# Optimization experiments

Hardware: AMD Instinct MI355X
Metric: run time of the kernel (lower is better)

The kernel has to match this reference:

```python
import jax, jax.numpy as jnp
import numpy as np

D_MODEL = 2048
N_HEADS = 16
HEAD_DIM = D_MODEL // N_HEADS
ROPE_BASE = 10000.0


def rope(x):
    # x: [b, h, s, d]; matches the torch module exactly:
    # x1 = even dims, x2 = odd dims; output = concat([x1*cos - x2*sin, x1*sin + x2*cos], -1)
    b, h, s, d = x.shape
    theta = 1.0 / ROPE_BASE ** (jnp.arange(0, d, 2, dtype=jnp.float32) / d)  # [d/2]
    angles = jnp.arange(s, dtype=jnp.float32)[:, None] * theta[None, :]       # [s, d/2]
    cos = jnp.cos(angles)[None, None]  # [1,1,s,d/2]
    sin = jnp.sin(angles)[None, None]
    x1, x2 = x[..., ::2], x[..., 1::2]
    return jnp.concatenate([x1 * cos - x2 * sin, x1 * sin + x2 * cos], axis=-1)


def setup_inputs() -> dict:
    key = jax.random.key(0)
    ks = jax.random.split(key, 5)
    b, s = 2, 2048
    x = jax.random.normal(ks[0], (b, s, D_MODEL), dtype=jnp.float32)
    scale_in = 1.0 / np.sqrt(D_MODEL)
    Wqkv = jax.random.normal(ks[1], (D_MODEL, 3 * D_MODEL), dtype=jnp.float32) * scale_in
    bqkv = jnp.zeros((3 * D_MODEL,), dtype=jnp.float32)
    Wo = jax.random.normal(ks[2], (D_MODEL, D_MODEL), dtype=jnp.float32) * scale_in
    bo = jnp.zeros((D_MODEL,), dtype=jnp.float32)
    return {"x": x, "Wqkv": Wqkv, "bqkv": bqkv, "Wo": Wo, "bo": bo}


def reference(x, Wqkv, bqkv, Wo, bo):
    b, s, d = x.shape
    qkv = x @ Wqkv + bqkv                      # [b, s, 3d]
    q, k, v = jnp.split(qkv, 3, axis=-1)
    def to_heads(t):
        return t.reshape(b, s, N_HEADS, HEAD_DIM).transpose(0, 2, 1, 3)  # [b,h,s,hd]
    q, k, v = to_heads(q), to_heads(k), to_heads(v)
    q = rope(q)
    k = rope(k)
    scores = jnp.einsum('bhqd,bhkd->bhqk', q, k) / jnp.sqrt(jnp.float32(HEAD_DIM))
    attn = jax.nn.softmax(scores, axis=-1)
    out = jnp.einsum('bhqk,bhkd->bhqd', attn, v)
    out = out.transpose(0, 2, 1, 3).reshape(b, s, d)
    return out @ Wo + bo
```

## Files before the change

kernel.cpp:

```cpp
#include <hip/hip_runtime.h>
#include <hip/hip_bf16.h>
#include <cstdint>
#include <type_traits>

#define D_MODEL 2048
#define NH 16
#define HD 128
#define SEQ 2048
#define QKV_LD (3 * D_MODEL)

typedef __attribute__((ext_vector_type(8))) short short8;
typedef __attribute__((ext_vector_type(4))) float f32x4;
typedef __attribute__((ext_vector_type(16))) float f32x16;

__device__ __forceinline__ ushort f2bf(float f) {
    union { float f; uint32_t u; } c; c.f = f;
    uint32_t u = c.u;
    uint32_t r = (u + 0x7FFFu + ((u >> 16) & 1u)) >> 16;
    return (ushort)r;
}
__device__ __forceinline__ float bf2f(ushort b) {
    union { uint32_t u; float f; } c; c.u = ((uint32_t)b) << 16;
    return c.f;
}

__device__ __forceinline__ void load_lds16(const ushort* g, ushort* l) {
    __builtin_amdgcn_global_load_lds(
        (const __attribute__((address_space(1))) void*)g,
        (__attribute__((address_space(3))) void*)l, 16, 0, 0);
}

#define WAITV(N) asm volatile("s_waitcnt vmcnt(" #N ")" ::: "memory")
#define BARF()   do { __builtin_amdgcn_s_barrier(); \
                      asm volatile("" ::: "memory"); } while (0)
#define PRIO1    __builtin_amdgcn_s_setprio(1)
#define PRIO0    __builtin_amdgcn_s_setprio(0)

__global__ void cvt_bf16_kernel(const float* __restrict__ in, ushort* __restrict__ out, int n4) {
    int idx = blockIdx.x * blockDim.x + threadIdx.x;
    if (idx >= n4) return;
    float4 v = ((const float4*)in)[idx];
    ushort4 o;
    o.x = f2bf(v.x); o.y = f2bf(v.y); o.z = f2bf(v.z); o.w = f2bf(v.w);
    ((ushort4*)out)[idx] = o;
}

__global__ void transpose_bf16_kernel(const float* __restrict__ in, ushort* __restrict__ out,
                                      int R, int C) {
    __shared__ float tile[32][33];
    int tx = threadIdx.x, ty = threadIdx.y;
    int c0 = blockIdx.x * 32, r0 = blockIdx.y * 32;
    for (int i = 0; i < 4; ++i) {
        int r = r0 + ty + i * 8;
        tile[ty + i * 8][tx] = in[(size_t)r * C + c0 + tx];
    }
    __syncthreads();
    for (int i = 0; i < 4; ++i) {
        int c = c0 + ty + i * 8;
        out[(size_t)c * R + r0 + tx] = f2bf(tile[tx][ty + i * 8]);
    }
}

#define B_ROWOFF(L) (NHALF == 2 ? (((L) & 1) * 128 + ((L) >> 1) * 32) : ((L) * 64))
#define STAGE_A(L, T_, B_) load_lds16(Ag + (size_t)(L) * 64 * K + (size_t)(T_) * 64, \
                                      smA + (B_) * 16384 + (L) * 4096 + ldsW)
#define STAGE_B(L, T_, B_) load_lds16(Bg + (size_t)B_ROWOFF(L) * K + (size_t)(T_) * 64, \
                                      smB + (B_) * (8192 * NHALF) + (L) * 4096 + ldsW)
#define READ_A(MH) do { const ushort* _ab = smA + cb * 16384 + aRow + (MH) * 4096; \
    _Pragma("unroll") for (int i_ = 0; i_ < 4; ++i_) { \
        af[i_][0] = *(const short8*)(_ab + i_ * 1024 + pc0); \
        af[i_][1] = *(const short8*)(_ab + i_ * 1024 + pc1); } } while (0)
#define READ_BH(dst, NHh) do { const ushort* _bb = smB + cb * (8192 * NHALF) + (NHh) * 8192 + bRow; \
    _Pragma("unroll") for (int j_ = 0; j_ < 2; ++j_) { \
        dst[j_][0] = *(const short8*)(_bb + j_ * 1024 + pc0); \
        dst[j_][1] = *(const short8*)(_bb + j_ * 1024 + pc1); } } while (0)
#define MFMA_PH(MH, NHh, bf) do { \
    _Pragma("unroll") for (int i_ = 0; i_ < 4; ++i_) \
    _Pragma("unroll") for (int j_ = 0; j_ < 2; ++j_) { \
        acc[(MH) * 4 + i_][(NHh) * 2 + j_] = __builtin_amdgcn_mfma_f32_16x16x32_bf16( \
            af[i_][0], bf[j_][0], acc[(MH) * 4 + i_][(NHh) * 2 + j_], 0, 0, 0); \
        acc[(MH) * 4 + i_][(NHh) * 2 + j_] = __builtin_amdgcn_mfma_f32_16x16x32_bf16( \
            af[i_][1], bf[j_][1], acc[(MH) * 4 + i_][(NHh) * 2 + j_], 0, 0, 0); } } while (0)

template <typename OutT, int NHALF>
__global__ __launch_bounds__(512, 2) void gemm256(
    const ushort* __restrict__ A,
    const ushort* __restrict__ Bt,
    const float* __restrict__ bias,
    OutT* __restrict__ C,
    int M, int N, int K)
{
    __shared__ __align__(16) ushort sm[32768 + 2 * 8192 * NHALF];
    ushort* smA = sm;
    ushort* smB = sm + 32768;

    int t = threadIdx.x;
    int w = t >> 6, lane = t & 63;
    int lr = lane & 15, lh = lane >> 4;
    int wm_idx = w >> 2, wn_idx = w & 3;
    int m0 = blockIdx.y * 256, n0 = blockIdx.x * (128 * NHALF);

    int srow = t >> 3;
    int scol = ((t & 7) ^ (srow & 7)) << 3;
    const ushort* Ag = A + (size_t)(m0 + srow) * K + scol;
    int bq = (NHALF == 2) ? ((srow >> 5) * 64 + (srow & 31)) : srow;
    const ushort* Bg = Bt + (size_t)(n0 + bq) * K + scol;
    int ldsW = w * 512;

    int pc0 = (lh ^ (lr & 7)) << 3;
    int pc1 = ((4 + lh) ^ (lr & 7)) << 3;
    int aRow = (wm_idx * 128 + lr) * 64;
    int bRow = (wn_idx * 32 + lr) * 64;

    f32x4 acc[8][2 * NHALF];
#pragma unroll
    for (int i = 0; i < 8; ++i)
#pragma unroll
        for (int j = 0; j < 2 * NHALF; ++j) acc[i][j] = (f32x4)0.0f;
    short8 af[4][2], bf0[2][2], bf1[2][2];

    int NT = K >> 6;

    if constexpr (NHALF == 2) {
        STAGE_A(0, 0, 0); STAGE_A(2, 0, 0); STAGE_B(0, 0, 0); STAGE_B(1, 0, 0);
        STAGE_B(2, 0, 0); STAGE_B(3, 0, 0);
        STAGE_A(1, 0, 0); STAGE_A(3, 0, 0);
        WAITV(4);
    } else {
        STAGE_A(0, 0, 0); STAGE_A(2, 0, 0); STAGE_B(0, 0, 0);
        STAGE_B(1, 0, 0); STAGE_A(1, 0, 0); STAGE_A(3, 0, 0);
        WAITV(2);
    }
    BARF();

    for (int T = 0; T < NT; ++T) {
        int cb = T & 1, nb = cb ^ 1;
        bool pf = (T + 1 < NT);
        if constexpr (NHALF == 2) {
            READ_A(0); READ_BH(bf0, 0);
            if (pf) { STAGE_A(0, T + 1, nb); STAGE_A(2, T + 1, nb);
                      STAGE_B(0, T + 1, nb); STAGE_B(1, T + 1, nb); }
            BARF();
            PRIO1; MFMA_PH(0, 0, bf0); PRIO0;
            if (pf) WAITV(6); else WAITV(2);
            BARF();
            READ_BH(bf1, 1);
            if (pf) { STAGE_B(2, T + 1, nb); STAGE_B(3, T + 1, nb); }
            BARF();
            PRIO1; MFMA_PH(0, 1, bf1); PRIO0;
            if (pf) WAITV(6); else WAITV(0);
            BARF();
            READ_A(1);
            if (pf) { STAGE_A(1, T + 1, nb); STAGE_A(3, T + 1, nb); }
            BARF();
            PRIO1; MFMA_PH(1, 1, bf1); MFMA_PH(1, 0, bf0); PRIO0;
            if (pf) WAITV(4);
            BARF();
        } else {
            READ_A(0); READ_BH(bf0, 0);
            if (pf) { STAGE_A(0, T + 1, nb); STAGE_A(2, T + 1, nb); STAGE_B(0, T + 1, nb); }
            BARF();
            PRIO1; MFMA_PH(0, 0, bf0); PRIO0;
            if (pf) WAITV(3); else WAITV(0);
            BARF();
            READ_A(1);
            if (pf) { STAGE_B(1, T + 1, nb); STAGE_A(1, T + 1, nb); STAGE_A(3, T + 1, nb); }
            BARF();
            PRIO1; MFMA_PH(1, 0, bf0); PRIO0;
            if (pf) WAITV(2);
            BARF();
        }
    }

    float bv[2 * NHALF];
#pragma unroll
    for (int jj = 0; jj < 2 * NHALF; ++jj) bv[jj] = bias[n0 + wn_idx * 32 * NHALF + jj * 16 + lr];
#pragma unroll
    for (int ii = 0; ii < 8; ++ii) {
        int row = m0 + wm_idx * 128 + ii * 16 + lh * 4;
#pragma unroll
        for (int jj = 0; jj < 2 * NHALF; ++jj) {
            int col = n0 + wn_idx * 32 * NHALF + jj * 16 + lr;
#pragma unroll
            for (int r = 0; r < 4; ++r) {
                float v = acc[ii][jj][r] + bv[jj];
                if constexpr (std::is_same<OutT, ushort>::value)
                    C[(size_t)(row + r) * N + col] = f2bf(v);
                else
                    C[(size_t)(row + r) * N + col] = v;
            }
        }
    }
}

#define STAGE_A3(L, T_, B_) load_lds16(Ag + (size_t)(L) * 64 * K + (size_t)(T_) * 64, \
                                       smA + (B_) * 8192 + (L) * 4096 + ldsW)
#define STAGE_B3(L, T_, B_) load_lds16(Bg + (size_t)((((L) & 1) * 2 + wnp) * 96 + ((L) >> 1) * 32 + rb) * K + (size_t)(T_) * 64, \
                                       smB + (B_) * 24576 + (L) * 4096 + ldsW)
#define READ_A3() do { const ushort* _ab = smA + cb * 8192 + aRow; \
    _Pragma("unroll") for (int i_ = 0; i_ < 4; ++i_) { \
        af[i_][0] = *(const short8*)(_ab + i_ * 1024 + pc0); \
        af[i_][1] = *(const short8*)(_ab + i_ * 1024 + pc1); } } while (0)
#define READ_B3(H) do { const ushort* _bb = smB + cb * 24576 + (H) * 8192 + bRow; \
    _Pragma("unroll") for (int j_ = 0; j_ < 2; ++j_) { \
        bfr[j_][0] = *(const short8*)(_bb + j_ * 1024 + pc0); \
        bfr[j_][1] = *(const short8*)(_bb + j_ * 1024 + pc1); } } while (0)
#define MFMA_P3(H) do { \
    _Pragma("unroll") for (int i_ = 0; i_ < 4; ++i_) \
    _Pragma("unroll") for (int j_ = 0; j_ < 2; ++j_) { \
        acc[i_][(H) * 2 + j_] = __builtin_amdgcn_mfma_f32_16x16x32_bf16( \
            af[i_][0], bfr[j_][0], acc[i_][(H) * 2 + j_], 0, 0, 0); \
        acc[i_][(H) * 2 + j_] = __builtin_amdgcn_mfma_f32_16x16x32_bf16( \
            af[i_][1], bfr[j_][1], acc[i_][(H) * 2 + j_], 0, 0, 0); } } while (0)

__global__ __launch_bounds__(512, 2) void gemm384(
    const ushort* __restrict__ A,
    const ushort* __restrict__ Bt,
    const float* __restrict__ bias,
    ushort* __restrict__ C,
    int M, int N, int K)
{
    __shared__ __align__(16) ushort sm[65536];
    ushort* smA = sm;
    ushort* smB = sm + 16384;

    int t = threadIdx.x;
    int w = t >> 6, lane = t & 63;
    int lr = lane & 15, lh = lane >> 4;
    int wm_idx = w >> 2, wn_idx = w & 3;
    int m0 = blockIdx.y * 128, n0 = blockIdx.x * 384;

    int srow = t >> 3;
    int scol = ((t & 7) ^ (srow & 7)) << 3;
    const ushort* Ag = A + (size_t)(m0 + srow) * K + scol;
    const ushort* Bg = Bt + (size_t)n0 * K + scol;
    int wnp = srow >> 5;
    int rb = srow & 31;
    int ldsW = w * 512;

    int pc0 = (lh ^ (lr & 7)) << 3;
    int pc1 = ((4 + lh) ^ (lr & 7)) << 3;
    int aRow = (wm_idx * 64 + lr) * 64;
    int bRow = (wn_idx * 32 + lr) * 64;

    f32x4 acc[4][6];
#pragma unroll
    for (int i = 0; i < 4; ++i)
#pragma unroll
        for (int j = 0; j < 6; ++j) acc[i][j] = (f32x4)0.0f;
    short8 af[4][2], bfr[2][2];

    int NT = K >> 6;

    STAGE_A3(0, 0, 0); STAGE_A3(1, 0, 0); STAGE_B3(0, 0, 0); STAGE_B3(1, 0, 0);
    STAGE_B3(2, 0, 0); STAGE_B3(3, 0, 0); STAGE_B3(4, 0, 0); STAGE_B3(5, 0, 0);
    WAITV(4);
    BARF();

    for (int T = 0; T < NT; ++T) {
        int cb = T & 1, nb = cb ^ 1;
        bool pf = (T + 1 < NT);
        READ_A3(); READ_B3(0);
        if (pf) { STAGE_A3(0, T + 1, nb); STAGE_A3(1, T + 1, nb); STAGE_B3(0, T + 1, nb); }
        BARF();
        PRIO1; MFMA_P3(0); PRIO0;
        if (pf) WAITV(5); else WAITV(2);
        BARF();
        READ_B3(1);
        if (pf) { STAGE_B3(1, T + 1, nb); STAGE_B3(2, T + 1, nb); STAGE_B3(3, T + 1, nb); }
        BARF();
        PRIO1; MFMA_P3(1); PRIO0;
        if (pf) WAITV(6); else WAITV(0);
        BARF();
        READ_B3(2);
        if (pf) { STAGE_B3(4, T + 1, nb); STAGE_B3(5, T + 1, nb); }
        BARF();
        PRIO1; MFMA_P3(2); PRIO0;
        if (pf) WAITV(4);
        BARF();
    }

    float bv[6];
#pragma unroll
    for (int jj = 0; jj < 6; ++jj) bv[jj] = bias[n0 + wn_idx * 96 + jj * 16 + lr];
#pragma unroll
    for (int ii = 0; ii < 4; ++ii) {
        int row = m0 + wm_idx * 64 + ii * 16 + lh * 4;
#pragma unroll
        for (int jj = 0; jj < 6; ++jj) {
            int col = n0 + wn_idx * 96 + jj * 16 + lr;
#pragma unroll
            for (int r = 0; r < 4; ++r) {
                float v = acc[ii][jj][r] + bv[jj];
                C[(size_t)(row + r) * N + col] = f2bf(v);
            }
        }
    }
}

__global__ void rope_table(float2* __restrict__ tab) {
    int i = blockIdx.x * blockDim.x + threadIdx.x;
    int s = i >> 6, j = i & 63;
    float theta = powf(10000.0f, -(float)j * (1.0f / 64.0f));
    float ang = (float)s * theta;
    float sn, cs;
    sincosf(ang, &sn, &cs);
    tab[i] = make_float2(cs, sn);
}

__global__ void rope_cast_qk(const ushort* __restrict__ qkv,
                             const float2* __restrict__ tab,
                             ushort* __restrict__ Qb, ushort* __restrict__ Kb) {
    int t = threadIdx.x;
    int wv = blockIdx.x * 4 + (t >> 6);
    int j = t & 63;
    int bs = wv >> 5;
    int rem = wv & 31;
    int which = rem >> 4;
    int h = rem & 15;
    int s = bs & 2047;
    int b = bs >> 11;
    size_t src = (size_t)bs * QKV_LD + which * D_MODEL + h * HD;
    uint32_t pr = *(const uint32_t*)(qkv + src + 2 * j);
    float x1 = bf2f((ushort)(pr & 0xffff));
    float x2 = bf2f((ushort)(pr >> 16));
    float2 cspair = tab[(s << 6) + j];
    float cs = cspair.x, sn = cspair.y;
    float sc = which ? 1.0f : 0.08838834764831845f;
    float o1 = (x1 * cs - x2 * sn) * sc;
    float o2 = (x1 * sn + x2 * cs) * sc;
    ushort* dst = which ? Kb : Qb;
    size_t obase = ((size_t)(b * NH + h) * SEQ + s) * HD;
    dst[obase + j] = f2bf(o1);
    dst[obase + 64 + j] = f2bf(o2);
}

__global__ void v_transpose(const ushort* __restrict__ qkv, ushort* __restrict__ Vt) {
    __shared__ ushort tile[32][33];
    int tx = threadIdx.x, ty = threadIdx.y;
    int s0 = blockIdx.x * 32;
    int d0 = blockIdx.y * 32;
    int bh = blockIdx.z;
    int b = bh >> 4, h = bh & 15;
    for (int i = 0; i < 4; ++i) {
        int s = s0 + ty + i * 8;
        tile[ty + i * 8][tx] = qkv[((size_t)(b * SEQ + s)) * QKV_LD + 2 * D_MODEL + h * HD + d0 + tx];
    }
    __syncthreads();
    for (int i = 0; i < 4; ++i) {
        int d = d0 + ty + i * 8;
        Vt[((size_t)bh * HD + d) * SEQ + s0 + tx] = tile[tx][ty + i * 8];
    }
}

__global__ __launch_bounds__(256) void attn_mfma(const ushort* __restrict__ Qb,
                                                 const ushort* __restrict__ Kb,
                                                 const ushort* __restrict__ Vt,
                                                 ushort* __restrict__ ctx) {
    __shared__ ushort smem[25600];
    ushort* Ks = smem;
    ushort* Vts = smem + 8192;
    ushort* Ps = smem + 16384;

    int t = threadIdx.x;
    int w = t >> 6, l = t & 63;
    int l31 = l & 31, g = l >> 5;
    int q0 = blockIdx.x * 128;
    int bh = blockIdx.y;
    int b = bh >> 4, h = bh & 15;

    int qrow = q0 + w * 32 + l31;
    const ushort* Qg = Qb + ((size_t)bh * SEQ + qrow) * HD;
    short8 qf[8];
#pragma unroll
    for (int kc = 0; kc < 8; kc++)
        qf[kc] = *(const short8*)(Qg + kc * 16 + g * 8);

    f32x16 O[4];
#pragma unroll
    for (int di = 0; di < 4; di++) O[di] = (f32x16)0.0f;
    float m_run = -INFINITY, l_run = 0.0f;

    const ushort* KgB = Kb + (size_t)bh * SEQ * HD;
    const ushort* VtB = Vt + (size_t)bh * HD * SEQ;

    for (int k0 = 0; k0 < SEQ; k0 += 64) {
        __syncthreads();
#pragma unroll
        for (int c2 = 0; c2 < 4; c2++) {
            int f = c2 * 256 + t;
            int r = f >> 4, c = f & 15;
            int cp = c ^ (r & 15);
            uint4 v = *(const uint4*)(KgB + (size_t)(k0 + r) * HD + c * 8);
            *(uint4*)(Ks + r * 128 + cp * 8) = v;
        }
#pragma unroll
        for (int c2 = 0; c2 < 4; c2++) {
            int f = c2 * 256 + t;
            int d = f >> 3, c = f & 7;
            int cp = c ^ (d & 7);
            uint4 v = *(const uint4*)(VtB + (size_t)d * SEQ + k0 + c * 8);
            *(uint4*)(Vts + d * 64 + cp * 8) = v;
        }
        __syncthreads();

        f32x16 St[2];
        St[0] = (f32x16)0.0f;
        St[1] = (f32x16)0.0f;
        PRIO1;
#pragma unroll
        for (int ki = 0; ki < 2; ki++) {
            int row = ki * 32 + l31;
#pragma unroll
            for (int kc = 0; kc < 8; kc++) {
                int cp = (kc * 2 + g) ^ (row & 15);
                short8 a = *(const short8*)(Ks + row * 128 + cp * 8);
                St[ki] = __builtin_amdgcn_mfma_f32_32x32x16_bf16(a, qf[kc], St[ki], 0, 0, 0);
            }
        }
        PRIO0;

        float mx = -INFINITY;
#pragma unroll
        for (int ki = 0; ki < 2; ki++)
#pragma unroll
            for (int r = 0; r < 16; r++) mx = fmaxf(mx, St[ki][r]);
        mx = fmaxf(mx, __shfl_xor(mx, 32));
        float mn = fmaxf(m_run, mx);
        float alpha = __expf(m_run - mn);
        m_run = mn;
        float psum = 0.0f;
#pragma unroll
        for (int ki = 0; ki < 2; ki++)
#pragma unroll
            for (int r = 0; r < 16; r++) {
                float p = __expf(St[ki][r] - mn);
                St[ki][r] = p;
                psum += p;
            }
        psum += __shfl_xor(psum, 32);
        l_run = l_run * alpha + psum;
#pragma unroll
        for (int di = 0; di < 4; di++)
#pragma unroll
            for (int r = 0; r < 16; r++) O[di][r] *= alpha;

        {
            int qloc = w * 32 + l31;
            ushort* Pr = Ps + qloc * 72;
#pragma unroll
            for (int ki = 0; ki < 2; ki++)
#pragma unroll
                for (int u = 0; u < 4; u++) {
                    ushort4 pk;
                    pk.x = f2bf(St[ki][4 * u + 0]);
                    pk.y = f2bf(St[ki][4 * u + 1]);
                    pk.z = f2bf(St[ki][4 * u + 2]);
                    pk.w = f2bf(St[ki][4 * u + 3]);
                    *(ushort4*)(Pr + ki * 32 + 8 * u + 4 * g) = pk;
                }
        }

        {
            int qloc = w * 32 + l31;
            short8 pb[4];
#pragma unroll
            for (int kc = 0; kc < 4; kc++)
                pb[kc] = *(const short8*)(Ps + qloc * 72 + kc * 16 + g * 8);
            PRIO1;
#pragma unroll
            for (int di = 0; di < 4; di++) {
                int d = di * 32 + l31;
#pragma unroll
                for (int kc = 0; kc < 4; kc++) {
                    int cp = (kc * 2 + g) ^ (d & 7);
                    short8 va = *(const short8*)(Vts + d * 64 + cp * 8);
                    O[di] = __builtin_amdgcn_mfma_f32_32x32x16_bf16(va, pb[kc], O[di], 0, 0, 0);
                }
            }
            PRIO0;
        }
    }

    __syncthreads();
    float inv = 1.0f / l_run;
    ushort* ob = smem;
    {
        int qloc = w * 32 + l31;
        ushort* orow = ob + qloc * 128;
#pragma unroll
        for (int di = 0; di < 4; di++)
#pragma unroll
            for (int u = 0; u < 4; u++) {
                ushort4 pk;
                pk.x = f2bf(O[di][4 * u + 0] * inv);
                pk.y = f2bf(O[di][4 * u + 1] * inv);
                pk.z = f2bf(O[di][4 * u + 2] * inv);
                pk.w = f2bf(O[di][4 * u + 3] * inv);
                *(ushort4*)(orow + di * 32 + 8 * u + 4 * g) = pk;
            }
    }
#pragma unroll
    for (int p = 0; p < 8; p++) {
        int qloc = w * 32 + p * 4 + (l >> 4);
        int c16 = l & 15;
        uint4 v = *(const uint4*)(ob + qloc * 128 + c16 * 8);
        size_t tok = (size_t)b * SEQ + q0 + qloc;
        *(uint4*)(ctx + tok * D_MODEL + h * HD + c16 * 8) = v;
    }
}

extern "C" void kernel_launch(void* const* d_in, const int* in_sizes, int n_in,
                              void* d_out, int out_size, void* d_ws, size_t ws_size,
                              hipStream_t stream) {
    const float* x    = (const float*)d_in[0];
    const float* Wqkv = (const float*)d_in[1];
    const float* bqkv = (const float*)d_in[2];
    const float* Wo   = (const float*)d_in[3];
    const float* bo   = (const float*)d_in[4];
    float* out = (float*)d_out;

    char* ws = (char*)d_ws;
    ushort* x_bf   = (ushort*)(ws);
    ushort* wqkvT  = (ushort*)(ws + 16777216);
    ushort* woT    = (ushort*)(ws + 41943040);
    ushort* qkv_bf = (ushort*)(ws + 50331648);
    ushort* Qb     = (ushort*)(ws + 100663296);
    ushort* Kb     = (ushort*)(ws + 117440512);
    ushort* VtG    = (ushort*)(ws + 134217728);
    ushort* ctx    = (ushort*)(ws + 150994944);
    float2* rtab   = (float2*)(ws + 150994944);

    rope_table<<<512, 256, 0, stream>>>(rtab);
    cvt_bf16_kernel<<<8192, 256, 0, stream>>>(x, x_bf, 2097152);
    transpose_bf16_kernel<<<dim3(192, 64), dim3(32, 8), 0, stream>>>(Wqkv, wqkvT, 2048, 6144);
    transpose_bf16_kernel<<<dim3(64, 64), dim3(32, 8), 0, stream>>>(Wo, woT, 2048, 2048);
    gemm384<<<dim3(16, 32), 512, 0, stream>>>(x_bf, wqkvT, bqkv, qkv_bf, 4096, 6144, 2048);
    rope_cast_qk<<<32768, 256, 0, stream>>>(qkv_bf, rtab, Qb, Kb);
    v_transpose<<<dim3(64, 4, 32), dim3(32, 8), 0, stream>>>(qkv_bf, VtG);
    attn_mfma<<<dim3(16, 32), 256, 0, stream>>>(Qb, Kb, VtG, ctx);
    gemm256<float, 1><<<dim3(16, 16), 512, 0, stream>>>(ctx, woT, bo, out, 4096, 2048, 2048);
}
```

Before: 423.4 us.

## Merge prep and rope/V kernels into fused launches, remap attention blocks, drop setprio

Merges the four preprocessing launches (rope table, x cast, two weight transposes) into one kernel that dispatches on block index. Likewise merges the rope/cast and V-transpose kernels into one launch. Remaps attention workgroup IDs so consecutive blocks are spread across heads, presumably for XCD/L2 locality, and removes the s_setprio hints around the MFMA loops. The goal is to cut launch overhead and tail gaps between small kernels, at the cost of divergent heterogeneous blocks sharing one launch configuration.

```diff
diff --git a/kernel.cpp b/kernel.cpp
--- a/kernel.cpp
+++ b/kernel.cpp
@@ -36,20 +36,12 @@
 #define PRIO1    __builtin_amdgcn_s_setprio(1)
 #define PRIO0    __builtin_amdgcn_s_setprio(0)
 
-__global__ void cvt_bf16_kernel(const float* __restrict__ in, ushort* __restrict__ out, int n4) {
-    int idx = blockIdx.x * blockDim.x + threadIdx.x;
-    if (idx >= n4) return;
-    float4 v = ((const float4*)in)[idx];
-    ushort4 o;
-    o.x = f2bf(v.x); o.y = f2bf(v.y); o.z = f2bf(v.z); o.w = f2bf(v.w);
-    ((ushort4*)out)[idx] = o;
-}
-
-__global__ void transpose_bf16_kernel(const float* __restrict__ in, ushort* __restrict__ out,
-                                      int R, int C) {
-    __shared__ float tile[32][33];
-    int tx = threadIdx.x, ty = threadIdx.y;
-    int c0 = blockIdx.x * 32, r0 = blockIdx.y * 32;
+__device__ __forceinline__ void transpose_body(const float* __restrict__ in,
+                                               ushort* __restrict__ out,
+                                               int R, int C, int bx, int by, int t,
+                                               float (*tile)[33]) {
+    int tx = t & 31, ty = t >> 5;
+    int c0 = bx * 32, r0 = by * 32;
     for (int i = 0; i < 4; ++i) {
         int r = r0 + ty + i * 8;
         tile[ty + i * 8][tx] = in[(size_t)r * C + c0 + tx];
@@ -58,6 +50,36 @@
     for (int i = 0; i < 4; ++i) {
         int c = c0 + ty + i * 8;
         out[(size_t)c * R + r0 + tx] = f2bf(tile[tx][ty + i * 8]);
+    }
+}
+
+__global__ void prep_fused(const float* __restrict__ x, ushort* __restrict__ x_bf,
+                           const float* __restrict__ Wqkv, ushort* __restrict__ wqkvT,
+                           const float* __restrict__ Wo, ushort* __restrict__ woT,
+                           float2* __restrict__ rtab) {
+    __shared__ float tile[32][33];
+    int blk = blockIdx.x;
+    int t = threadIdx.x;
+    if (blk < 512) {
+        int i = blk * 256 + t;
+        int s = i >> 6, j = i & 63;
+        float theta = powf(10000.0f, -(float)j * (1.0f / 64.0f));
+        float ang = (float)s * theta;
+        float sn, cs;
+        sincosf(ang, &sn, &cs);
+        rtab[i] = make_float2(cs, sn);
+    } else if (blk < 8704) {
+        int idx = (blk - 512) * 256 + t;
+        float4 v = ((const float4*)x)[idx];
+        ushort4 o;
+        o.x = f2bf(v.x); o.y = f2bf(v.y); o.z = f2bf(v.z); o.w = f2bf(v.w);
+        ((ushort4*)x_bf)[idx] = o;
+    } else if (blk < 20992) {
+        int i = blk - 8704;
+        transpose_body(Wqkv, wqkvT, 2048, 6144, i % 192, i / 192, t, tile);
+    } else {
+        int i = blk - 20992;
+        transpose_body(Wo, woT, 2048, 2048, i & 63, i >> 6, t, tile);
     }
 }
 
@@ -298,58 +320,51 @@
     }
 }
 
-__global__ void rope_table(float2* __restrict__ tab) {
-    int i = blockIdx.x * blockDim.x + threadIdx.x;
-    int s = i >> 6, j = i & 63;
-    float theta = powf(10000.0f, -(float)j * (1.0f / 64.0f));
-    float ang = (float)s * theta;
-    float sn, cs;
-    sincosf(ang, &sn, &cs);
-    tab[i] = make_float2(cs, sn);
-}
-
-__global__ void rope_cast_qk(const ushort* __restrict__ qkv,
-                             const float2* __restrict__ tab,
-                             ushort* __restrict__ Qb, ushort* __restrict__ Kb) {
+__global__ void rope_v_fused(const ushort* __restrict__ qkv, const float2* __restrict__ tab,
+                             ushort* __restrict__ Qb, ushort* __restrict__ Kb,
+                             ushort* __restrict__ Vt) {
+    __shared__ ushort tile[32][33];
+    int blk = blockIdx.x;
     int t = threadIdx.x;
-    int wv = blockIdx.x * 4 + (t >> 6);
-    int j = t & 63;
-    int bs = wv >> 5;
-    int rem = wv & 31;
-    int which = rem >> 4;
-    int h = rem & 15;
-    int s = bs & 2047;
-    int b = bs >> 11;
-    size_t src = (size_t)bs * QKV_LD + which * D_MODEL + h * HD;
-    uint32_t pr = *(const uint32_t*)(qkv + src + 2 * j);
-    float x1 = bf2f((ushort)(pr & 0xffff));
-    float x2 = bf2f((ushort)(pr >> 16));
-    float2 cspair = tab[(s << 6) + j];
-    float cs = cspair.x, sn = cspair.y;
-    float sc = which ? 1.0f : 0.08838834764831845f;
-    float o1 = (x1 * cs - x2 * sn) * sc;
-    float o2 = (x1 * sn + x2 * cs) * sc;
-    ushort* dst = which ? Kb : Qb;
-    size_t obase = ((size_t)(b * NH + h) * SEQ + s) * HD;
-    dst[obase + j] = f2bf(o1);
-    dst[obase + 64 + j] = f2bf(o2);
-}
-
-__global__ void v_transpose(const ushort* __restrict__ qkv, ushort* __restrict__ Vt) {
-    __shared__ ushort tile[32][33];
-    int tx = threadIdx.x, ty = threadIdx.y;
-    int s0 = blockIdx.x * 32;
-    int d0 = blockIdx.y * 32;
-    int bh = blockIdx.z;
-    int b = bh >> 4, h = bh & 15;
-    for (int i = 0; i < 4; ++i) {
-        int s = s0 + ty + i * 8;
-        tile[ty + i * 8][tx] = qkv[((size_t)(b * SEQ + s)) * QKV_LD + 2 * D_MODEL + h * HD + d0 + tx];
-    }
-    __syncthreads();
-    for (int i = 0; i < 4; ++i) {
-        int d = d0 + ty + i * 8;
-        Vt[((size_t)bh * HD + d) * SEQ + s0 + tx] = tile[tx][ty + i * 8];
+    if (blk < 32768) {
+        int wv = blk * 4 + (t >> 6);
+        int j = t & 63;
+        int bs = wv >> 5;
+        int rem = wv & 31;
+        int which = rem >> 4;
+        int h = rem & 15;
+        int s = bs & 2047;
+        int b = bs >> 11;
+        size_t src = (size_t)bs * QKV_LD + which * D_MODEL + h * HD;
+        uint32_t pr = *(const uint32_t*)(qkv + src + 2 * j);
+        float x1 = bf2f((ushort)(pr & 0xffff));
+        float x2 = bf2f((ushort)(pr >> 16));
+        float2 cspair = tab[(s << 6) + j];
+        float cs = cspair.x, sn = cspair.y;
+        float sc = which ? 1.0f : 0.08838834764831845f;
+        float o1 = (x1 * cs - x2 * sn) * sc;
+        float o2 = (x1 * sn + x2 * cs) * sc;
+        ushort* dst = which ? Kb : Qb;
+        size_t obase = ((size_t)(b * NH + h) * SEQ + s) * HD;
+        dst[obase + j] = f2bf(o1);
+        dst[obase + 64 + j] = f2bf(o2);
+    } else {
+        int i = blk - 32768;
+        int bx = i & 63, by = (i >> 6) & 3, bz = i >> 8;
+        int tx = t & 31, ty = t >> 5;
+        int s0 = bx * 32;
+        int d0 = by * 32;
+        int bh = bz;
+        int b = bh >> 4, h = bh & 15;
+        for (int k = 0; k < 4; ++k) {
+            int s = s0 + ty + k * 8;
+            tile[ty + k * 8][tx] = qkv[((size_t)(b * SEQ + s)) * QKV_LD + 2 * D_MODEL + h * HD + d0 + tx];
+        }
+        __syncthreads();
+        for (int k = 0; k < 4; ++k) {
+            int d = d0 + ty + k * 8;
+            Vt[((size_t)bh * HD + d) * SEQ + s0 + tx] = tile[tx][ty + k * 8];
+        }
     }
 }
 
@@ -365,8 +380,10 @@
     int t = threadIdx.x;
     int w = t >> 6, l = t & 63;
     int l31 = l & 31, g = l >> 5;
-    int q0 = blockIdx.x * 128;
-    int bh = blockIdx.y;
+    int flat = blockIdx.y * 16 + blockIdx.x;
+    int wid = (flat & 7) * 64 + (flat >> 3);
+    int q0 = (wid & 15) * 128;
+    int bh = wid >> 4;
     int b = bh >> 4, h = bh & 15;
 
     int qrow = q0 + w * 32 + l31;
@@ -407,7 +424,6 @@
         f32x16 St[2];
         St[0] = (f32x16)0.0f;
         St[1] = (f32x16)0.0f;
-        PRIO1;
 #pragma unroll
         for (int ki = 0; ki < 2; ki++) {
             int row = ki * 32 + l31;
@@ -418,7 +434,6 @@
                 St[ki] = __builtin_amdgcn_mfma_f32_32x32x16_bf16(a, qf[kc], St[ki], 0, 0, 0);
             }
         }
-        PRIO0;
 
         float mx = -INFINITY;
 #pragma unroll
@@ -467,7 +482,6 @@
 #pragma unroll
             for (int kc = 0; kc < 4; kc++)
                 pb[kc] = *(const short8*)(Ps + qloc * 72 + kc * 16 + g * 8);
-            PRIO1;
 #pragma unroll
             for (int di = 0; di < 4; di++) {
                 int d = di * 32 + l31;
@@ -478,7 +492,6 @@
                     O[di] = __builtin_amdgcn_mfma_f32_32x32x16_bf16(va, pb[kc], O[di], 0, 0, 0);
                 }
             }
-            PRIO0;
         }
     }
 
@@ -531,13 +544,9 @@
     ushort* ctx    = (ushort*)(ws + 150994944);
     float2* rtab   = (float2*)(ws + 150994944);
 
-    rope_table<<<512, 256, 0, stream>>>(rtab);
-    cvt_bf16_kernel<<<8192, 256, 0, stream>>>(x, x_bf, 2097152);
-    transpose_bf16_kernel<<<dim3(192, 64), dim3(32, 8), 0, stream>>>(Wqkv, wqkvT, 2048, 6144);
-    transpose_bf16_kernel<<<dim3(64, 64), dim3(32, 8), 0, stream>>>(Wo, woT, 2048, 2048);
+    prep_fused<<<25088, 256, 0, stream>>>(x, x_bf, Wqkv, wqkvT, Wo, woT, rtab);
     gemm384<<<dim3(16, 32), 512, 0, stream>>>(x_bf, wqkvT, bqkv, qkv_bf, 4096, 6144, 2048);
-    rope_cast_qk<<<32768, 256, 0, stream>>>(qkv_bf, rtab, Qb, Kb);
-    v_transpose<<<dim3(64, 4, 32), dim3(32, 8), 0, stream>>>(qkv_bf, VtG);
+    rope_v_fused<<<40960, 256, 0, stream>>>(qkv_bf, rtab, Qb, Kb, VtG);
     attn_mfma<<<dim3(16, 32), 256, 0, stream>>>(Qb, Kb, VtG, ctx);
     gemm256<float, 1><<<dim3(16, 16), 512, 0, stream>>>(ctx, woT, bo, out, 4096, 2048, 2048);
 }
```

After: 408.2 us (median of 2 runs). 3.6% less time.
